# Kernel optimization log

Measured on AMD Instinct MI355X. Metric: run time of the kernel, lower is better.

Reference implementation:

```python
import jax, jax.numpy as jnp
import numpy as np

N_NODES = 100000
N_EDGES = 800000
HID = 64
FIN = 6


def _add_self_loops(src, dst, w, n):
    loop = jnp.arange(n, dtype=src.dtype)
    return (jnp.concatenate([src, loop]),
            jnp.concatenate([dst, loop]),
            jnp.concatenate([w, jnp.ones((n,), dtype=w.dtype)]))


def _gcn_conv(x, W, b, src, dst, norm):
    # x: [N,F]; W: [F,H]. PyG GCNConv: transform, then normalized scatter-add, then bias.
    h = x @ W                                     # [N,H]
    msg = norm[:, None] * h[src]                  # [E',H] gathered messages
    agg = jax.ops.segment_sum(msg, dst, num_segments=x.shape[0])
    return agg + b


def setup_inputs() -> dict:
    key = jax.random.key(0)
    ks = jax.random.split(key, 8)
    vertex_features = jax.random.normal(ks[0], (N_NODES, FIN), dtype=jnp.float32)
    edges = jax.random.randint(ks[1], (2, N_EDGES), 0, N_NODES, dtype=jnp.int64 if jax.config.jax_enable_x64 else jnp.int32)
    weights = jax.random.uniform(ks[2], (N_EDGES,), dtype=jnp.float32)

    def glorot(k, shape):
        lim = np.sqrt(6.0 / (shape[0] + shape[1]))
        return jax.random.uniform(k, shape, dtype=jnp.float32, minval=-lim, maxval=lim)

    inp = {
        'vertex_features': vertex_features,
        'edges': edges,
        'weights': weights,
        'W1': glorot(ks[3], (FIN, HID)), 'b1': jnp.zeros((HID,), jnp.float32),
        'W2': glorot(ks[4], (HID, HID)), 'b2': jnp.zeros((HID,), jnp.float32),
        'W3': glorot(ks[5], (HID, HID)), 'b3': jnp.zeros((HID,), jnp.float32),
        'W4': glorot(ks[6], (HID, HID)), 'b4': jnp.zeros((HID,), jnp.float32),
        'Wr': glorot(ks[7], (HID, 1)),   'br': jnp.zeros((1,), jnp.float32),
    }
    return inp


def reference(vertex_features, edges, weights, W1, b1, W2, b2, W3, b3, W4, b4, Wr, br):
    n = vertex_features.shape[0]
    src, dst = edges[0], edges[1]
    src, dst, w = _add_self_loops(src, dst, weights, n)
    # symmetric normalization D^{-1/2} A_hat D^{-1/2}
    deg = jax.ops.segment_sum(w, dst, num_segments=n)
    dinv = jnp.where(deg > 0, jax.lax.rsqrt(deg), 0.0)
    norm = dinv[src] * w * dinv[dst]

    x = vertex_features
    for W, b in ((W1, b1), (W2, b2), (W3, b3), (W4, b4)):
        x = jax.nn.relu(_gcn_conv(x, W, b, src, dst, norm))
    pooled = jnp.max(x, axis=0)                   # global max pool, batch=None -> [H]
    out = pooled @ Wr + br                        # [1]
    return jnp.squeeze(out)
```

## Files before the change

### kernel.cpp

```cpp
#include <hip/hip_runtime.h>
#include <hip/hip_fp16.h>
#include <math.h>


__global__ void init_kernel(int* counts, float* pooled, int N) {
    int i = blockIdx.x * blockDim.x + threadIdx.x;
    if (i < N) counts[i] = 0;
    if (i < 64) pooled[i] = 0.0f;
}

__global__ void count_slot_kernel(const int* __restrict__ dst, int* counts, int* eslot, int E) {
    int e = blockIdx.x * blockDim.x + threadIdx.x;
    if (e >= E) return;
    eslot[e] = atomicAdd(&counts[dst[e]], 1);
}

__global__ void scan1_kernel(const int* __restrict__ counts, int* bsums, int N) {
    __shared__ int s[256];
    int t = threadIdx.x, i = blockIdx.x * 256 + t;
    s[t] = (i < N) ? counts[i] : 0;
    __syncthreads();
    for (int o = 128; o > 0; o >>= 1) {
        if (t < o) s[t] += s[t + o];
        __syncthreads();
    }
    if (t == 0) bsums[blockIdx.x] = s[0];
}

__global__ void scan2_kernel(int* bsums, int nb) {
    __shared__ int s[512];
    int t = threadIdx.x;
    int v = (t < nb) ? bsums[t] : 0;
    s[t] = v; __syncthreads();
    for (int o = 1; o < 512; o <<= 1) {
        int x = (t >= o) ? s[t - o] : 0;
        __syncthreads();
        s[t] += x;
        __syncthreads();
    }
    if (t < nb) bsums[t] = s[t] - v;
}

__global__ void scan3_kernel(const int* __restrict__ counts, const int* __restrict__ bsums,
                             int* rowptr, int N) {
    __shared__ int s[256];
    int t = threadIdx.x, i = blockIdx.x * 256 + t;
    int v = (i < N) ? counts[i] : 0;
    s[t] = v; __syncthreads();
    for (int o = 1; o < 256; o <<= 1) {
        int x = (t >= o) ? s[t - o] : 0;
        __syncthreads();
        s[t] += x;
        __syncthreads();
    }
    if (i <= N) rowptr[i] = bsums[blockIdx.x] + s[t] - v;
}

__global__ void fill2_kernel(const int* __restrict__ src, const int* __restrict__ dst,
                             const float* __restrict__ w, const int* __restrict__ rowptr,
                             const int* __restrict__ eslot, int* colsrc, float* wcsr, int E) {
    int e = blockIdx.x * blockDim.x + threadIdx.x;
    if (e >= E) return;
    int p = rowptr[dst[e]] + eslot[e];
    colsrc[p] = src[e];
    wcsr[p] = w[e];
}

__global__ void degdinv_kernel(const float* __restrict__ wcsr, const int* __restrict__ rowptr,
                               float* dinv, int N) {
    int i = blockIdx.x * blockDim.x + threadIdx.x;
    if (i >= N) return;
    float d = 1.0f;
    int jb = rowptr[i], je = rowptr[i + 1];
    for (int j = jb; j < je; ++j) d += wcsr[j];
    dinv[i] = 1.0f / sqrtf(d);
}

__global__ void norm_kernel(const int* __restrict__ rowptr, const int* __restrict__ colsrc,
                            const float* __restrict__ dinv, float* wcsr, int N) {
    int i = blockIdx.x * blockDim.x + threadIdx.x;
    if (i >= N) return;
    float dn = dinv[i];
    int jb = rowptr[i], je = rowptr[i + 1];
    for (int j = jb; j < je; ++j)
        wcsr[j] = dinv[colsrc[j]] * wcsr[j] * dn;
}

__global__ void gather6_kernel(const float* __restrict__ x, const int* __restrict__ rowptr,
                               const int* __restrict__ colsrc, const float* __restrict__ normcsr,
                               const float* __restrict__ dinv, float* __restrict__ g, int N) {
    int i = blockIdx.x * blockDim.x + threadIdx.x;
    if (i >= N) return;
    float dn = dinv[i];
    float sc = dn * dn;
    float acc[6];
    {
        const float2* xr = (const float2*)(x + (size_t)i * 6);
        float2 a = xr[0], bv = xr[1], c = xr[2];
        acc[0] = sc * a.x; acc[1] = sc * a.y; acc[2] = sc * bv.x;
        acc[3] = sc * bv.y; acc[4] = sc * c.x; acc[5] = sc * c.y;
    }
    int jb = rowptr[i], je = rowptr[i + 1];
    for (int j = jb; j < je; ++j) {
        int s = colsrc[j];
        float nm = normcsr[j];
        const float2* xr = (const float2*)(x + (size_t)s * 6);
        float2 a = xr[0], bv = xr[1], c = xr[2];
        acc[0] = fmaf(nm, a.x, acc[0]); acc[1] = fmaf(nm, a.y, acc[1]);
        acc[2] = fmaf(nm, bv.x, acc[2]); acc[3] = fmaf(nm, bv.y, acc[3]);
        acc[4] = fmaf(nm, c.x, acc[4]); acc[5] = fmaf(nm, c.y, acc[5]);
    }
#pragma unroll
    for (int f = 0; f < 6; ++f) g[(size_t)i * 6 + f] = acc[f];
}

__global__ void gather64_kernel(const __half* __restrict__ h, const int* __restrict__ rowptr,
                                const int* __restrict__ colsrc, const float* __restrict__ normcsr,
                                const float* __restrict__ dinv, float* __restrict__ agg, int N) {
    int wid = blockIdx.x * (blockDim.x >> 6) + (threadIdx.x >> 6);
    if (wid >= N) return;
    int lane = threadIdx.x & 63;
    int g = lane >> 4;
    int l16 = lane & 15;
    float4 acc = {0.f, 0.f, 0.f, 0.f};
    if (g == 0) {
        float dn = dinv[wid];
        float sc = dn * dn;
        uint2 r = ((const uint2*)(h + (size_t)wid * 64))[l16];
        __half2 p0 = *reinterpret_cast<__half2*>(&r.x);
        __half2 p1 = *reinterpret_cast<__half2*>(&r.y);
        float2 f0 = __half22float2(p0), f1 = __half22float2(p1);
        acc.x = sc * f0.x; acc.y = sc * f0.y; acc.z = sc * f1.x; acc.w = sc * f1.y;
    }
    int jb = rowptr[wid], je = rowptr[wid + 1];
    for (int j = jb + g; j < je; j += 4) {
        int s = colsrc[j];
        float nm = normcsr[j];
        uint2 r = ((const uint2*)(h + (size_t)s * 64))[l16];
        __half2 p0 = *reinterpret_cast<__half2*>(&r.x);
        __half2 p1 = *reinterpret_cast<__half2*>(&r.y);
        float2 f0 = __half22float2(p0), f1 = __half22float2(p1);
        acc.x = fmaf(nm, f0.x, acc.x);
        acc.y = fmaf(nm, f0.y, acc.y);
        acc.z = fmaf(nm, f1.x, acc.z);
        acc.w = fmaf(nm, f1.y, acc.w);
    }
#pragma unroll
    for (int o = 16; o <= 32; o <<= 1) {
        acc.x += __shfl_xor(acc.x, o);
        acc.y += __shfl_xor(acc.y, o);
        acc.z += __shfl_xor(acc.z, o);
        acc.w += __shfl_xor(acc.w, o);
    }
    if (g == 0) ((float4*)(agg + (size_t)wid * 64))[l16] = acc;
}

__global__ void __launch_bounds__(256)
__attribute__((amdgpu_waves_per_eu(2, 4)))
mm64_kernel(const float* __restrict__ xin, const float* __restrict__ W,
            const float* __restrict__ b, __half* __restrict__ h, int N) {
    __shared__ float xl[64 * 68];
    __shared__ float Wt[64 * 68];
    const int tid = threadIdx.x;
    const long nb = (long)blockIdx.x * 64;

#pragma unroll
    for (int r = 0; r < 4; ++r) {
        int q = tid + 256 * r;
        int row = q >> 4, c4 = q & 15;
        ((float4*)&Wt[row * 68 + c4 * 4])[0] = ((const float4*)W)[q];
        long n = nb + row;
        float4 v = {0.f, 0.f, 0.f, 0.f};
        if (n < N) v = ((const float4*)(xin + n * 64))[c4];
        ((float4*)&xl[row * 68 + c4 * 4])[0] = v;
    }
    __syncthreads();

    const int tx = tid & 15;
    const int ty = tid >> 4;

    float4 acc0 = {0,0,0,0}, acc1 = {0,0,0,0}, acc2 = {0,0,0,0}, acc3 = {0,0,0,0};
#pragma unroll 4
    for (int kc = 0; kc < 16; ++kc) {
        float4 w0 = *(const float4*)&Wt[(kc * 4 + 0) * 68 + tx * 4];
        float4 w1 = *(const float4*)&Wt[(kc * 4 + 1) * 68 + tx * 4];
        float4 w2 = *(const float4*)&Wt[(kc * 4 + 2) * 68 + tx * 4];
        float4 w3 = *(const float4*)&Wt[(kc * 4 + 3) * 68 + tx * 4];
        float4 x0 = *(const float4*)&xl[(ty * 4 + 0) * 68 + kc * 4];
        float4 x1 = *(const float4*)&xl[(ty * 4 + 1) * 68 + kc * 4];
        float4 x2 = *(const float4*)&xl[(ty * 4 + 2) * 68 + kc * 4];
        float4 x3 = *(const float4*)&xl[(ty * 4 + 3) * 68 + kc * 4];
#define MMSTEP(A, X) \
        A.x = fmaf(X.x, w0.x, A.x); A.y = fmaf(X.x, w0.y, A.y); A.z = fmaf(X.x, w0.z, A.z); A.w = fmaf(X.x, w0.w, A.w); \
        A.x = fmaf(X.y, w1.x, A.x); A.y = fmaf(X.y, w1.y, A.y); A.z = fmaf(X.y, w1.z, A.z); A.w = fmaf(X.y, w1.w, A.w); \
        A.x = fmaf(X.z, w2.x, A.x); A.y = fmaf(X.z, w2.y, A.y); A.z = fmaf(X.z, w2.z, A.z); A.w = fmaf(X.z, w2.w, A.w); \
        A.x = fmaf(X.w, w3.x, A.x); A.y = fmaf(X.w, w3.y, A.y); A.z = fmaf(X.w, w3.z, A.z); A.w = fmaf(X.w, w3.w, A.w);
        MMSTEP(acc0, x0) MMSTEP(acc1, x1) MMSTEP(acc2, x2) MMSTEP(acc3, x3)
#undef MMSTEP
    }

    float4 vb = ((const float4*)b)[tx];
#define MMOUT(A, I) { \
        long n = nb + ty * 4 + I; \
        if (n < N) { \
            float o0 = fmaxf(A.x + vb.x, 0.f), o1 = fmaxf(A.y + vb.y, 0.f); \
            float o2 = fmaxf(A.z + vb.z, 0.f), o3 = fmaxf(A.w + vb.w, 0.f); \
            __half2 p0 = __floats2half2_rn(o0, o1), p1 = __floats2half2_rn(o2, o3); \
            uint2 pk; pk.x = *(unsigned int*)&p0; pk.y = *(unsigned int*)&p1; \
            ((uint2*)(h + n * 64))[tx] = pk; \
        } }
    MMOUT(acc0, 0) MMOUT(acc1, 1) MMOUT(acc2, 2) MMOUT(acc3, 3)
#undef MMOUT
}

__global__ void __launch_bounds__(256)
mm6_kernel(const float* __restrict__ xin, const float* __restrict__ W,
           const float* __restrict__ b, __half* __restrict__ h, int N) {
    long idx = (long)blockIdx.x * blockDim.x + threadIdx.x;
    if (idx >= (long)N * 64) return;
    long n = idx >> 6;
    int c = (int)(idx & 63);
    const float* xr = xin + n * 6;
    float a = b[c];
    a = fmaf(xr[0], W[0 * 64 + c], a);
    a = fmaf(xr[1], W[1 * 64 + c], a);
    a = fmaf(xr[2], W[2 * 64 + c], a);
    a = fmaf(xr[3], W[3 * 64 + c], a);
    a = fmaf(xr[4], W[4 * 64 + c], a);
    a = fmaf(xr[5], W[5 * 64 + c], a);
    h[idx] = __float2half(fmaxf(a, 0.0f));
}

__global__ void pool_kernel(const __half* __restrict__ x, float* pooled, int N) {
    int lane = threadIdx.x & 63;
    int wid = blockIdx.x * (blockDim.x >> 6) + (threadIdx.x >> 6);
    int nw = gridDim.x * (blockDim.x >> 6);
    float m = 0.0f;
    for (int n = wid; n < N; n += nw)
        m = fmaxf(m, __half2float(x[(size_t)n * 64 + lane]));
    atomicMax((unsigned int*)&pooled[lane], __float_as_uint(m));
}

__global__ void out_kernel(const float* __restrict__ pooled, const float* __restrict__ Wr,
                           const float* __restrict__ br, float* out) {
    int lane = threadIdx.x;
    float v = pooled[lane] * Wr[lane];
    for (int o = 32; o > 0; o >>= 1) v += __shfl_xor(v, o);
    if (lane == 0) out[0] = v + br[0];
}

extern "C" void kernel_launch(void* const* d_in, const int* in_sizes, int n_in,
                              void* d_out, int out_size, void* d_ws, size_t ws_size,
                              hipStream_t stream) {
    const float* vf = (const float*)d_in[0];
    const int* edges = (const int*)d_in[1];
    const float* w = (const float*)d_in[2];
    const float* W1 = (const float*)d_in[3];  const float* b1 = (const float*)d_in[4];
    const float* W2 = (const float*)d_in[5];  const float* b2 = (const float*)d_in[6];
    const float* W3 = (const float*)d_in[7];  const float* b3 = (const float*)d_in[8];
    const float* W4 = (const float*)d_in[9];  const float* b4 = (const float*)d_in[10];
    const float* Wr = (const float*)d_in[11]; const float* br = (const float*)d_in[12];
    float* out = (float*)d_out;

    const int FIN = 6;
    const int N = in_sizes[0] / FIN;
    const int E = in_sizes[2];
    const int* src = edges;
    const int* dst = edges + E;

    char* p = (char*)d_ws;
    float*  dinv    = (float*)p;   p += (size_t)N * 4;
    int*    rowptr  = (int*)p;     p += (size_t)(N + 1) * 4;
    int*    counts  = (int*)p;     p += (size_t)N * 4;
    int*    eslot   = (int*)p;     p += (size_t)E * 4;
    int*    colsrc  = (int*)p;     p += (size_t)E * 4;
    float*  wcsr    = (float*)p;   p += (size_t)E * 4;
    float*  g6      = (float*)p;   p += (size_t)N * 6 * 4;
    __half* h16     = (__half*)p;  p += (size_t)N * 64 * 2;
    float*  agg     = (float*)p;   p += (size_t)N * 64 * 4;
    float*  pooled  = (float*)p;   p += 64 * 4;
    int*    bsums   = (int*)p;     p += 512 * 4;

    const int nbN = (N + 255) / 256;
    const int nbE = (E + 255) / 256;
    const int nbW = (N + 3) / 4;
    const int nbG = (N + 63) / 64;
    const int nbM6 = (int)(((long)N * 64 + 255) / 256);

    init_kernel<<<nbN, 256, 0, stream>>>(counts, pooled, N);
    count_slot_kernel<<<nbE, 256, 0, stream>>>(dst, counts, eslot, E);
    scan1_kernel<<<nbN, 256, 0, stream>>>(counts, bsums, N);
    scan2_kernel<<<1, 512, 0, stream>>>(bsums, nbN);
    scan3_kernel<<<nbN, 256, 0, stream>>>(counts, bsums, rowptr, N);
    fill2_kernel<<<nbE, 256, 0, stream>>>(src, dst, w, rowptr, eslot, colsrc, wcsr, E);
    degdinv_kernel<<<nbN, 256, 0, stream>>>(wcsr, rowptr, dinv, N);
    norm_kernel<<<nbN, 256, 0, stream>>>(rowptr, colsrc, dinv, wcsr, N);

    gather6_kernel<<<nbN, 256, 0, stream>>>(vf, rowptr, colsrc, wcsr, dinv, g6, N);
    mm6_kernel<<<nbM6, 256, 0, stream>>>(g6, W1, b1, h16, N);
    gather64_kernel<<<nbW, 256, 0, stream>>>(h16, rowptr, colsrc, wcsr, dinv, agg, N);
    mm64_kernel<<<nbG, 256, 0, stream>>>(agg, W2, b2, h16, N);
    gather64_kernel<<<nbW, 256, 0, stream>>>(h16, rowptr, colsrc, wcsr, dinv, agg, N);
    mm64_kernel<<<nbG, 256, 0, stream>>>(agg, W3, b3, h16, N);
    gather64_kernel<<<nbW, 256, 0, stream>>>(h16, rowptr, colsrc, wcsr, dinv, agg, N);
    mm64_kernel<<<nbG, 256, 0, stream>>>(agg, W4, b4, h16, N);

    pool_kernel<<<256, 256, 0, stream>>>(h16, pooled, N);
    out_kernel<<<1, 64, 0, stream>>>(pooled, Wr, br, out);
}
```

Measured before the change: 332.4 us.

## Fuse neighbor gather into 64-wide matmul kernel and fold max-pool into last layer

Each 64-wide layer's sparse gather-aggregate is moved into the matmul kernel. The aggregated rows are written straight into shared memory, so the fp32 agg buffer no longer round-trips through global memory and a launch per layer is saved. Gather parallelism changes from one 64-lane wave per node with 4 edge groups to 8 threads per node walking all edges serially. The last layer reduces ReLU-max per block and uses atomicMax into pooled instead of writing h and running a separate pool kernel, and ping-pong fp16 buffers are used.

Measured after the change: 351.4 us. 1.06x slower.

```diff
diff --git a/kernel.cpp b/kernel.cpp
--- a/kernel.cpp
+++ b/kernel.cpp
@@ -114,51 +114,32 @@
     for (int f = 0; f < 6; ++f) g[(size_t)i * 6 + f] = acc[f];
 }
 
-__global__ void gather64_kernel(const __half* __restrict__ h, const int* __restrict__ rowptr,
-                                const int* __restrict__ colsrc, const float* __restrict__ normcsr,
-                                const float* __restrict__ dinv, float* __restrict__ agg, int N) {
-    int wid = blockIdx.x * (blockDim.x >> 6) + (threadIdx.x >> 6);
-    if (wid >= N) return;
-    int lane = threadIdx.x & 63;
-    int g = lane >> 4;
-    int l16 = lane & 15;
-    float4 acc = {0.f, 0.f, 0.f, 0.f};
-    if (g == 0) {
-        float dn = dinv[wid];
-        float sc = dn * dn;
-        uint2 r = ((const uint2*)(h + (size_t)wid * 64))[l16];
-        __half2 p0 = *reinterpret_cast<__half2*>(&r.x);
-        __half2 p1 = *reinterpret_cast<__half2*>(&r.y);
-        float2 f0 = __half22float2(p0), f1 = __half22float2(p1);
-        acc.x = sc * f0.x; acc.y = sc * f0.y; acc.z = sc * f1.x; acc.w = sc * f1.y;
-    }
-    int jb = rowptr[wid], je = rowptr[wid + 1];
-    for (int j = jb + g; j < je; j += 4) {
-        int s = colsrc[j];
-        float nm = normcsr[j];
-        uint2 r = ((const uint2*)(h + (size_t)s * 64))[l16];
-        __half2 p0 = *reinterpret_cast<__half2*>(&r.x);
-        __half2 p1 = *reinterpret_cast<__half2*>(&r.y);
-        float2 f0 = __half22float2(p0), f1 = __half22float2(p1);
-        acc.x = fmaf(nm, f0.x, acc.x);
-        acc.y = fmaf(nm, f0.y, acc.y);
-        acc.z = fmaf(nm, f1.x, acc.z);
-        acc.w = fmaf(nm, f1.y, acc.w);
-    }
-#pragma unroll
-    for (int o = 16; o <= 32; o <<= 1) {
-        acc.x += __shfl_xor(acc.x, o);
-        acc.y += __shfl_xor(acc.y, o);
-        acc.z += __shfl_xor(acc.z, o);
-        acc.w += __shfl_xor(acc.w, o);
-    }
-    if (g == 0) ((float4*)(agg + (size_t)wid * 64))[l16] = acc;
-}
-
+__global__ void __launch_bounds__(256)
+mm6_kernel(const float* __restrict__ xin, const float* __restrict__ W,
+           const float* __restrict__ b, __half* __restrict__ h, int N) {
+    long idx = (long)blockIdx.x * blockDim.x + threadIdx.x;
+    if (idx >= (long)N * 64) return;
+    long n = idx >> 6;
+    int c = (int)(idx & 63);
+    const float* xr = xin + n * 6;
+    float a = b[c];
+    a = fmaf(xr[0], W[0 * 64 + c], a);
+    a = fmaf(xr[1], W[1 * 64 + c], a);
+    a = fmaf(xr[2], W[2 * 64 + c], a);
+    a = fmaf(xr[3], W[3 * 64 + c], a);
+    a = fmaf(xr[4], W[4 * 64 + c], a);
+    a = fmaf(xr[5], W[5 * 64 + c], a);
+    h[idx] = __float2half(fmaxf(a, 0.0f));
+}
+
+template<bool FUSE_POOL>
 __global__ void __launch_bounds__(256)
 __attribute__((amdgpu_waves_per_eu(2, 4)))
-mm64_kernel(const float* __restrict__ xin, const float* __restrict__ W,
-            const float* __restrict__ b, __half* __restrict__ h, int N) {
+gmm64_kernel(const __half* __restrict__ h_in, const int* __restrict__ rowptr,
+             const int* __restrict__ colsrc, const float* __restrict__ normcsr,
+             const float* __restrict__ dinv,
+             const float* __restrict__ W, const float* __restrict__ b,
+             __half* __restrict__ h_out, float* pooled, int N) {
     __shared__ float xl[64 * 68];
     __shared__ float Wt[64 * 68];
     const int tid = threadIdx.x;
@@ -169,10 +150,44 @@
         int q = tid + 256 * r;
         int row = q >> 4, c4 = q & 15;
         ((float4*)&Wt[row * 68 + c4 * 4])[0] = ((const float4*)W)[q];
-        long n = nb + row;
-        float4 v = {0.f, 0.f, 0.f, 0.f};
-        if (n < N) v = ((const float4*)(xin + n * 64))[c4];
-        ((float4*)&xl[row * 68 + c4 * 4])[0] = v;
+    }
+
+    const int grp = tid >> 3;
+    const int l8 = tid & 7;
+#pragma unroll
+    for (int half = 0; half < 2; ++half) {
+        int row = half * 32 + grp;
+        long node = nb + row;
+        float4 accA = {0.f, 0.f, 0.f, 0.f};
+        float4 accB = {0.f, 0.f, 0.f, 0.f};
+        if (node < N) {
+            float dn = dinv[node];
+            float sc = dn * dn;
+            uint4 r = ((const uint4*)(h_in + node * 64))[l8];
+            __half2 p0 = *(__half2*)&r.x, p1 = *(__half2*)&r.y;
+            __half2 p2 = *(__half2*)&r.z, p3 = *(__half2*)&r.w;
+            float2 f0 = __half22float2(p0), f1 = __half22float2(p1);
+            float2 f2 = __half22float2(p2), f3 = __half22float2(p3);
+            accA.x = sc * f0.x; accA.y = sc * f0.y; accA.z = sc * f1.x; accA.w = sc * f1.y;
+            accB.x = sc * f2.x; accB.y = sc * f2.y; accB.z = sc * f3.x; accB.w = sc * f3.y;
+            int jb = rowptr[node], je = rowptr[node + 1];
+            for (int j = jb; j < je; ++j) {
+                int s = colsrc[j];
+                float nm = normcsr[j];
+                uint4 rr = ((const uint4*)(h_in + (size_t)s * 64))[l8];
+                __half2 q0 = *(__half2*)&rr.x, q1 = *(__half2*)&rr.y;
+                __half2 q2 = *(__half2*)&rr.z, q3 = *(__half2*)&rr.w;
+                float2 g0 = __half22float2(q0), g1 = __half22float2(q1);
+                float2 g2 = __half22float2(q2), g3 = __half22float2(q3);
+                accA.x = fmaf(nm, g0.x, accA.x); accA.y = fmaf(nm, g0.y, accA.y);
+                accA.z = fmaf(nm, g1.x, accA.z); accA.w = fmaf(nm, g1.y, accA.w);
+                accB.x = fmaf(nm, g2.x, accB.x); accB.y = fmaf(nm, g2.y, accB.y);
+                accB.z = fmaf(nm, g3.x, accB.z); accB.w = fmaf(nm, g3.y, accB.w);
+            }
+        }
+        float* dstp = &xl[row * 68 + l8 * 8];
+        ((float4*)dstp)[0] = accA;
+        ((float4*)dstp)[1] = accB;
     }
     __syncthreads();
 
@@ -200,6 +215,7 @@
     }
 
     float4 vb = ((const float4*)b)[tx];
+    if (!FUSE_POOL) {
 #define MMOUT(A, I) { \
         long n = nb + ty * 4 + I; \
         if (n < N) { \
@@ -207,38 +223,42 @@
             float o2 = fmaxf(A.z + vb.z, 0.f), o3 = fmaxf(A.w + vb.w, 0.f); \
             __half2 p0 = __floats2half2_rn(o0, o1), p1 = __floats2half2_rn(o2, o3); \
             uint2 pk; pk.x = *(unsigned int*)&p0; pk.y = *(unsigned int*)&p1; \
-            ((uint2*)(h + n * 64))[tx] = pk; \
+            ((uint2*)(h_out + n * 64))[tx] = pk; \
         } }
-    MMOUT(acc0, 0) MMOUT(acc1, 1) MMOUT(acc2, 2) MMOUT(acc3, 3)
+        MMOUT(acc0, 0) MMOUT(acc1, 1) MMOUT(acc2, 2) MMOUT(acc3, 3)
 #undef MMOUT
-}
-
-__global__ void __launch_bounds__(256)
-mm6_kernel(const float* __restrict__ xin, const float* __restrict__ W,
-           const float* __restrict__ b, __half* __restrict__ h, int N) {
-    long idx = (long)blockIdx.x * blockDim.x + threadIdx.x;
-    if (idx >= (long)N * 64) return;
-    long n = idx >> 6;
-    int c = (int)(idx & 63);
-    const float* xr = xin + n * 6;
-    float a = b[c];
-    a = fmaf(xr[0], W[0 * 64 + c], a);
-    a = fmaf(xr[1], W[1 * 64 + c], a);
-    a = fmaf(xr[2], W[2 * 64 + c], a);
-    a = fmaf(xr[3], W[3 * 64 + c], a);
-    a = fmaf(xr[4], W[4 * 64 + c], a);
-    a = fmaf(xr[5], W[5 * 64 + c], a);
-    h[idx] = __float2half(fmaxf(a, 0.0f));
-}
-
-__global__ void pool_kernel(const __half* __restrict__ x, float* pooled, int N) {
-    int lane = threadIdx.x & 63;
-    int wid = blockIdx.x * (blockDim.x >> 6) + (threadIdx.x >> 6);
-    int nw = gridDim.x * (blockDim.x >> 6);
-    float m = 0.0f;
-    for (int n = wid; n < N; n += nw)
-        m = fmaxf(m, __half2float(x[(size_t)n * 64 + lane]));
-    atomicMax((unsigned int*)&pooled[lane], __float_as_uint(m));
+    } else {
+        float4 m = {0.f, 0.f, 0.f, 0.f};
+#define MMMAX(A, I) { \
+        long n = nb + ty * 4 + I; \
+        if (n < N) { \
+            m.x = fmaxf(m.x, A.x + vb.x); m.y = fmaxf(m.y, A.y + vb.y); \
+            m.z = fmaxf(m.z, A.z + vb.z); m.w = fmaxf(m.w, A.w + vb.w); \
+        } }
+        MMMAX(acc0, 0) MMMAX(acc1, 1) MMMAX(acc2, 2) MMMAX(acc3, 3)
+#undef MMMAX
+        __syncthreads();
+        ((float4*)xl)[ty * 16 + tx] = m;
+        __syncthreads();
+#pragma unroll
+        for (int off = 8; off > 0; off >>= 1) {
+            if (ty < off) {
+                float4 a = ((float4*)xl)[ty * 16 + tx];
+                float4 c = ((float4*)xl)[(ty + off) * 16 + tx];
+                a.x = fmaxf(a.x, c.x); a.y = fmaxf(a.y, c.y);
+                a.z = fmaxf(a.z, c.z); a.w = fmaxf(a.w, c.w);
+                ((float4*)xl)[ty * 16 + tx] = a;
+            }
+            __syncthreads();
+        }
+        if (ty == 0) {
+            float4 m0 = ((float4*)xl)[tx];
+            atomicMax((unsigned int*)&pooled[tx * 4 + 0], __float_as_uint(m0.x));
+            atomicMax((unsigned int*)&pooled[tx * 4 + 1], __float_as_uint(m0.y));
+            atomicMax((unsigned int*)&pooled[tx * 4 + 2], __float_as_uint(m0.z));
+            atomicMax((unsigned int*)&pooled[tx * 4 + 3], __float_as_uint(m0.w));
+        }
+    }
 }
 
 __global__ void out_kernel(const float* __restrict__ pooled, const float* __restrict__ Wr,
@@ -276,14 +296,13 @@
     int*    colsrc  = (int*)p;     p += (size_t)E * 4;
     float*  wcsr    = (float*)p;   p += (size_t)E * 4;
     float*  g6      = (float*)p;   p += (size_t)N * 6 * 4;
-    __half* h16     = (__half*)p;  p += (size_t)N * 64 * 2;
-    float*  agg     = (float*)p;   p += (size_t)N * 64 * 4;
+    __half* hA      = (__half*)p;  p += (size_t)N * 64 * 2;
+    __half* hB      = (__half*)p;  p += (size_t)N * 64 * 2;
     float*  pooled  = (float*)p;   p += 64 * 4;
     int*    bsums   = (int*)p;     p += 512 * 4;
 
     const int nbN = (N + 255) / 256;
     const int nbE = (E + 255) / 256;
-    const int nbW = (N + 3) / 4;
     const int nbG = (N + 63) / 64;
     const int nbM6 = (int)(((long)N * 64 + 255) / 256);
 
@@ -297,14 +316,13 @@
     norm_kernel<<<nbN, 256, 0, stream>>>(rowptr, colsrc, dinv, wcsr, N);
 
     gather6_kernel<<<nbN, 256, 0, stream>>>(vf, rowptr, colsrc, wcsr, dinv, g6, N);
-    mm6_kernel<<<nbM6, 256, 0, stream>>>(g6, W1, b1, h16, N);
-    gather64_kernel<<<nbW, 256, 0, stream>>>(h16, rowptr, colsrc, wcsr, dinv, agg, N);
-    mm64_kernel<<<nbG, 256, 0, stream>>>(agg, W2, b2, h16, N);
-    gather64_kernel<<<nbW, 256, 0, stream>>>(h16, rowptr, colsrc, wcsr, dinv, agg, N);
-    mm64_kernel<<<nbG, 256, 0, stream>>>(agg, W3, b3, h16, N);
-    gather64_kernel<<<nbW, 256, 0, stream>>>(h16, rowptr, colsrc, wcsr, dinv, agg, N);
-    mm64_kernel<<<nbG, 256, 0, stream>>>(agg, W4, b4, h16, N);
-
-    pool_kernel<<<256, 256, 0, stream>>>(h16, pooled, N);
+    mm6_kernel<<<nbM6, 256, 0, stream>>>(g6, W1, b1, hA, N);
+    gmm64_kernel<false><<<nbG, 256, 0, stream>>>(hA, rowptr, colsrc, wcsr, dinv,
+                                                 W2, b2, hB, nullptr, N);
+    gmm64_kernel<false><<<nbG, 256, 0, stream>>>(hB, rowptr, colsrc, wcsr, dinv,
+                                                 W3, b3, hA, nullptr, N);
+    gmm64_kernel<true><<<nbG, 256, 0, stream>>>(hA, rowptr, colsrc, wcsr, dinv,
+                                                W4, b4, nullptr, pooled, N);
+
     out_kernel<<<1, 64, 0, stream>>>(pooled, Wr, br, out);
 }
```
